# Kernel tuning notes

Hardware: AMD Instinct MI355X
Metric: run time of the kernel (lower is better)

The kernel has to match this reference:

```python
import jax, jax.numpy as jnp
import numpy as np

D_MODEL = 1024
STATE_DIM = 256


def setup_inputs() -> dict:
    key = jax.random.key(0)
    k_u, k_lam, k_B, k_C = jax.random.split(key, 4)
    u = jax.random.normal(k_u, (4, 4096, D_MODEL), dtype=jnp.float32)
    # log_lambda ~ N(3.0, 0.5^2), matching torch.randn(state_dim)*0.5 + 3.0
    log_lambda = jax.random.normal(k_lam, (STATE_DIM,), dtype=jnp.float32) * 0.5 + 3.0
    # torch Linear weights: B.weight [state_dim, d_model], C.weight [d_model, state_dim]
    B_w = jax.random.normal(k_B, (STATE_DIM, D_MODEL), dtype=jnp.float32) / np.sqrt(D_MODEL)
    C_w = jax.random.normal(k_C, (D_MODEL, STATE_DIM), dtype=jnp.float32) / np.sqrt(STATE_DIM)
    D = jnp.zeros((D_MODEL,), dtype=jnp.float32)
    return {"u": u, "log_lambda": log_lambda, "B_w": B_w, "C_w": C_w, "D": D}


def reference(u, log_lambda, B_w, C_w, D):
    # u: [batch, seq, d_model]
    lam = jax.nn.sigmoid(log_lambda)                      # [state_dim]
    Bu = jnp.einsum('bsd,nd->bsn', u, B_w)                # [batch, seq, state_dim]

    def step(h, bu_t):
        h = lam * h + bu_t                                # [batch, state_dim]
        return h, h

    h0 = jnp.zeros((u.shape[0], lam.shape[0]), dtype=u.dtype)
    # scan over time axis; Bu transposed to [seq, batch, state_dim]
    _, hs = jax.lax.scan(step, h0, jnp.swapaxes(Bu, 0, 1))
    hs = jnp.swapaxes(hs, 0, 1)                           # [batch, seq, state_dim]
    y = jnp.einsum('bsn,dn->bsd', hs, C_w) + D * u        # [batch, seq, d_model]
    return y
```

## Files before the change

### kernel.cpp

```cpp
#include <hip/hip_runtime.h>
#include <math.h>

typedef unsigned short ushort_t;
typedef __bf16 v8bf __attribute__((ext_vector_type(8)));
typedef __bf16 v4bf __attribute__((ext_vector_type(4)));
typedef float  v4f  __attribute__((ext_vector_type(4)));
typedef float  f32x4 __attribute__((ext_vector_type(4)));

#define BATCH 4
#define SEQ 4096
#define DM 1024
#define NS 256
#define MROWS (BATCH*SEQ)

#define NCH 128
#define CL (SEQ/NCH)

#define BK 32
#define BK1 64

typedef __attribute__((address_space(1))) void as1_void;
typedef __attribute__((address_space(3))) void as3_void;

__device__ __forceinline__ void gl_lds16(const void* g, void* l) {
    __builtin_amdgcn_global_load_lds((as1_void*)g, (as3_void*)l, 16, 0, 0);
}

__device__ __forceinline__ ushort_t f2bf(float f) {
    unsigned u = __builtin_bit_cast(unsigned, f);
    u += 0x7fff + ((u >> 16) & 1);
    return (ushort_t)(u >> 16);
}

__device__ __forceinline__ float sigm(float x) { return 1.0f / (1.0f + expf(-x)); }

__device__ __forceinline__ float powk(int e, float l1, float l2, float l4,
                                      float l8, float l16) {
    float w = 1.0f;
    if (e & 1)  w *= l1;
    if (e & 2)  w *= l2;
    if (e & 4)  w *= l4;
    if (e & 8)  w *= l8;
    if (e & 16) w *= l16;
    return w;
}

__global__ __launch_bounds__(256)
void gemm1_fused(const float* __restrict__ A,
                 const ushort_t* __restrict__ B,
                 float* __restrict__ Bu,
                 const float* __restrict__ ll,
                 float* __restrict__ cf)
{
    const int K = DM;
    __shared__ __align__(16) ushort_t As[2][32*BK1];
    __shared__ __align__(16) ushort_t Bs[2][256*BK1];

    const int tid  = threadIdx.x;
    const int lane = tid & 63;
    const int wave = tid >> 6;
    const int m0   = blockIdx.x * 32;

    const int fr = lane & 15;
    const int fq = lane >> 4;

    int arow[2], ac4[2];
    #pragma unroll
    for (int j = 0; j < 2; ++j) {
        int cid = j*256 + tid;
        arow[j] = cid >> 4;
        ac4[j]  = (cid & 15) * 4;
    }
    int brow[8], bc[8];
    #pragma unroll
    for (int j = 0; j < 8; ++j) {
        int cid = j*256 + tid;
        brow[j] = cid >> 3;
        bc[j]   = (cid & 7) * 8;
    }

    f32x4 acc[2][4] = {};
    v4f areg[2];

    #pragma unroll
    for (int j = 0; j < 2; ++j)
        areg[j] = *(const v4f*)&A[(size_t)(m0 + arow[j])*K + ac4[j]];
    #pragma unroll
    for (int j = 0; j < 8; ++j)
        gl_lds16(&B[(size_t)brow[j]*K + bc[j]], &Bs[0][(j*256 + tid)*8]);

    const int NIT = K / BK1;
    for (int it = 0; it < NIT; ++it) {
        const int cur = it & 1;
        #pragma unroll
        for (int j = 0; j < 2; ++j)
            *(v4bf*)&As[cur][arow[j]*BK1 + ac4[j]] = __builtin_convertvector(areg[j], v4bf);
        __syncthreads();

        if (it + 1 < NIT) {
            const int k1 = (it + 1) * BK1;
            #pragma unroll
            for (int j = 0; j < 8; ++j)
                gl_lds16(&B[(size_t)brow[j]*K + k1 + bc[j]], &Bs[cur^1][(j*256 + tid)*8]);
            #pragma unroll
            for (int j = 0; j < 2; ++j)
                areg[j] = *(const v4f*)&A[(size_t)(m0 + arow[j])*K + k1 + ac4[j]];
        }

        #pragma unroll
        for (int kk = 0; kk < 2; ++kk) {
            v8bf af[2], bf[4];
            #pragma unroll
            for (int mi = 0; mi < 2; ++mi)
                af[mi] = *reinterpret_cast<const v8bf*>(
                    &As[cur][(mi*16 + fr)*BK1 + kk*32 + fq*8]);
            #pragma unroll
            for (int ni = 0; ni < 4; ++ni)
                bf[ni] = *reinterpret_cast<const v8bf*>(
                    &Bs[cur][(wave*64 + ni*16 + fr)*BK1 + kk*32 + fq*8]);

            #pragma unroll
            for (int mi = 0; mi < 2; ++mi)
                #pragma unroll
                for (int ni = 0; ni < 4; ++ni)
                    acc[mi][ni] = __builtin_amdgcn_mfma_f32_16x16x32_bf16(
                                      af[mi], bf[ni], acc[mi][ni], 0, 0, 0);
        }
    }

    #pragma unroll
    for (int mi = 0; mi < 2; ++mi) {
        #pragma unroll
        for (int ni = 0; ni < 4; ++ni) {
            const int col = wave*64 + ni*16 + fr;
            #pragma unroll
            for (int r = 0; r < 4; ++r)
                Bu[(size_t)(m0 + mi*16 + fq*4 + r)*NS + col] = acc[mi][ni][r];
        }
    }

    const int b_idx = m0 >> 12;
    const int c_idx = (m0 & 4095) >> 5;

    #pragma unroll
    for (int ni = 0; ni < 4; ++ni) {
        const int col = wave*64 + ni*16 + fr;
        const float l1  = sigm(ll[col]);
        const float l2  = l1*l1;
        const float l4  = l2*l2;
        const float l8  = l4*l4;
        const float l16 = l8*l8;
        float f = 0.0f;
        #pragma unroll
        for (int mi = 0; mi < 2; ++mi) {
            float w = powk(28 - mi*16 - fq*4, l1, l2, l4, l8, l16);
            f = fmaf(w, acc[mi][ni][3], f);
            w *= l1; f = fmaf(w, acc[mi][ni][2], f);
            w *= l1; f = fmaf(w, acc[mi][ni][1], f);
            w *= l1; f = fmaf(w, acc[mi][ni][0], f);
        }
        f += __shfl_xor(f, 16, 64);
        f += __shfl_xor(f, 32, 64);
        if (fq == 0)
            cf[((size_t)b_idx*NCH + c_idx)*NS + col] = f;
    }
}

__global__ __launch_bounds__(256)
void gemm2_mfma(const ushort_t* __restrict__ A,
                const ushort_t* __restrict__ B,
                float* __restrict__ C,
                const float* __restrict__ Dvec, const float* __restrict__ U)
{
    const int K = NS;
    const int N = DM;
    __shared__ __align__(16) ushort_t As[2][128*BK];
    __shared__ __align__(16) ushort_t Bs[2][128*BK];

    const int tid  = threadIdx.x;
    const int lane = tid & 63;
    const int wave = tid >> 6;
    const int wrow = wave >> 1;
    const int wcol = wave & 1;
    const int n0 = blockIdx.x * 128;
    const int m0 = blockIdx.y * 128;

    const int fr = lane & 15;
    const int fq = lane >> 4;

    f32x4 acc[4][4] = {};

    const int ch0 = wave*128 + lane;
    const int ch1 = ch0 + 64;
    const int r0 = ch0 >> 2, c0 = (ch0 & 3) * 8;
    const int r1 = ch1 >> 2, c1 = (ch1 & 3) * 8;

    gl_lds16(&A[(size_t)(m0 + r0)*K + c0], &As[0][ch0*8]);
    gl_lds16(&B[(size_t)(n0 + r0)*K + c0], &Bs[0][ch0*8]);
    gl_lds16(&A[(size_t)(m0 + r1)*K + c1], &As[0][ch1*8]);
    gl_lds16(&B[(size_t)(n0 + r1)*K + c1], &Bs[0][ch1*8]);

    for (int it = 0; it < K/BK; ++it) {
        const int cur = it & 1;
        __syncthreads();

        if (it + 1 < K/BK) {
            const int k1 = (it + 1) * BK;
            gl_lds16(&A[(size_t)(m0 + r0)*K + k1 + c0], &As[cur^1][ch0*8]);
            gl_lds16(&B[(size_t)(n0 + r0)*K + k1 + c0], &Bs[cur^1][ch0*8]);
            gl_lds16(&A[(size_t)(m0 + r1)*K + k1 + c1], &As[cur^1][ch1*8]);
            gl_lds16(&B[(size_t)(n0 + r1)*K + k1 + c1], &Bs[cur^1][ch1*8]);
        }

        v8bf af[4], bf[4];
        #pragma unroll
        for (int mi = 0; mi < 4; ++mi)
            af[mi] = *reinterpret_cast<const v8bf*>(&As[cur][(wrow*64 + mi*16 + fr)*BK + fq*8]);
        #pragma unroll
        for (int ni = 0; ni < 4; ++ni)
            bf[ni] = *reinterpret_cast<const v8bf*>(&Bs[cur][(wcol*64 + ni*16 + fr)*BK + fq*8]);

        #pragma unroll
        for (int mi = 0; mi < 4; ++mi)
            #pragma unroll
            for (int ni = 0; ni < 4; ++ni)
                acc[mi][ni] = __builtin_amdgcn_mfma_f32_16x16x32_bf16(
                                  af[mi], bf[ni], acc[mi][ni], 0, 0, 0);
    }

    const int orow = m0 + wrow*64 + (lane >> 4)*4;
    const int ocol = n0 + wcol*64 + (lane & 15);
    #pragma unroll
    for (int ni = 0; ni < 4; ++ni) {
        const int col = ocol + ni*16;
        const float d = Dvec[col];
        #pragma unroll
        for (int mi = 0; mi < 4; ++mi) {
            #pragma unroll
            for (int r = 0; r < 4; ++r) {
                const size_t idx = (size_t)(orow + mi*16 + r) * N + col;
                float v = acc[mi][ni][r];
                if (d != 0.0f) v = fmaf(d, U[idx], v);
                C[idx] = v;
            }
        }
    }
}

__global__ __launch_bounds__(256)
void cvt_w(const float4* __restrict__ Bw, const float4* __restrict__ Cw,
           ushort_t* __restrict__ Bo, ushort_t* __restrict__ Co)
{
    const int i = blockIdx.x * 256 + threadIdx.x;
    const float4* src = blockIdx.y ? Cw : Bw;
    ushort_t*     dst = blockIdx.y ? Co : Bo;
    float4 v = src[i];
    ushort4 o;
    o.x = f2bf(v.x); o.y = f2bf(v.y); o.z = f2bf(v.z); o.w = f2bf(v.w);
    *(ushort4*)&dst[4*(size_t)i] = o;
}

__global__ __launch_bounds__(256)
void scan_apply(const float* __restrict__ Bu, const float* __restrict__ ll,
                const float* __restrict__ cf, ushort_t* __restrict__ hs16)
{
    const int n = threadIdx.x, c = blockIdx.x, b = blockIdx.y;
    const float lam = sigm(ll[n]);
    float lamL = lam;
    #pragma unroll
    for (int i = 0; i < 5; ++i) lamL *= lamL;

    const float* cfb = cf + (size_t)b*NCH*NS + n;
    float x = 0.0f;
    for (int c0 = 0; c0 < c; c0 += 16) {
        float v[16];
        #pragma unroll
        for (int j = 0; j < 16; ++j) {
            const int cc = c0 + j;
            v[j] = (cc < c) ? cfb[(size_t)cc*NS] : 0.0f;
        }
        #pragma unroll
        for (int j = 0; j < 16; ++j) {
            if (c0 + j < c) x = fmaf(lamL, x, v[j]);
        }
    }

    const size_t base = ((size_t)b*SEQ + (size_t)c*CL)*NS + n;
    float v[CL];
    #pragma unroll
    for (int t = 0; t < CL; ++t)
        v[t] = Bu[base + (size_t)t*NS];

    float h = x;
    #pragma unroll
    for (int t = 0; t < CL; ++t) { h = fmaf(lam, h, v[t]); v[t] = h; }
    #pragma unroll
    for (int t = 0; t < CL; ++t) hs16[base + (size_t)t*NS] = f2bf(v[t]);
}

extern "C" void kernel_launch(void* const* d_in, const int* in_sizes, int n_in,
                              void* d_out, int out_size, void* d_ws, size_t ws_size,
                              hipStream_t stream) {
    const float* u          = (const float*)d_in[0];
    const float* log_lambda = (const float*)d_in[1];
    const float* B_w        = (const float*)d_in[2];
    const float* C_w        = (const float*)d_in[3];
    const float* Dv         = (const float*)d_in[4];
    float* y  = (float*)d_out;

    char* w = (char*)d_ws;
    float*    Bu    = (float*)w;
    ushort_t* hs16  = (ushort_t*)(w + 16777216);
    ushort_t* Bw16  = (ushort_t*)(w + 25165824);
    ushort_t* Cw16  = (ushort_t*)(w + 25690112);
    float*    cf    = (float*)(w + 26214400);

    dim3 blk(256);

    cvt_w<<<dim3(256, 2), blk, 0, stream>>>((const float4*)B_w, (const float4*)C_w,
                                            Bw16, Cw16);

    gemm1_fused<<<dim3(MROWS/32), blk, 0, stream>>>(u, Bw16, Bu, log_lambda, cf);

    scan_apply<<<dim3(NCH, BATCH), blk, 0, stream>>>(Bu, log_lambda, cf, hs16);

    gemm2_mfma<<<dim3(DM/128, MROWS/128), blk, 0, stream>>>(
        hs16, Cw16, y, Dv, u);
}
```

Baseline: 167.8 us.

## Fuse weight conversion, GEMM1 and chunked scan into one cooperative kernel

Merges the weight bf16 conversion, the first GEMM with chunk-carry computation, and the chunked scan into a single cooperative kernel that uses two grid-wide syncs. The Bu intermediate now stays in LDS instead of making a round trip through global memory. Tiles grow to 64 rows with 512 threads, and the LDS layouts are XOR-swizzled to reduce bank conflicts. The risks are grid-sync cost, the need for all 256 blocks to be co-resident, and heavier LDS use that lowers occupancy.

```diff
diff --git a/kernel.cpp b/kernel.cpp
--- a/kernel.cpp
+++ b/kernel.cpp
@@ -1,4 +1,5 @@
 #include <hip/hip_runtime.h>
+#include <hip/hip_cooperative_groups.h>
 #include <math.h>
 
 typedef unsigned short ushort_t;
@@ -16,8 +17,10 @@
 #define NCH 128
 #define CL (SEQ/NCH)
 
+#define BM1 64
+#define BK1 64
 #define BK 32
-#define BK1 64
+#define SST 258
 
 typedef __attribute__((address_space(1))) void as1_void;
 typedef __attribute__((address_space(3))) void as3_void;
@@ -45,38 +48,57 @@
     return w;
 }
 
-__global__ __launch_bounds__(256)
-void gemm1_fused(const float* __restrict__ A,
-                 const ushort_t* __restrict__ B,
-                 float* __restrict__ Bu,
-                 const float* __restrict__ ll,
-                 float* __restrict__ cf)
+__global__ __launch_bounds__(512)
+void fused1(const float* __restrict__ A,
+            const float* __restrict__ BwF,
+            const float* __restrict__ CwF,
+            ushort_t* __restrict__ Bw16,
+            ushort_t* __restrict__ Cw16,
+            const float* __restrict__ ll,
+            float* __restrict__ cf,
+            ushort_t* __restrict__ hs)
 {
     const int K = DM;
-    __shared__ __align__(16) ushort_t As[2][32*BK1];
-    __shared__ __align__(16) ushort_t Bs[2][256*BK1];
+    __shared__ __align__(16) union {
+        struct { ushort_t As[2][BM1*BK1]; ushort_t Bs[2][NS*BK1]; } g;
+        struct { float S[BM1*SST]; } s;
+    } L;
 
     const int tid  = threadIdx.x;
     const int lane = tid & 63;
     const int wave = tid >> 6;
-    const int m0   = blockIdx.x * 32;
-
+    const int wr = wave >> 2;
+    const int wc = wave & 3;
     const int fr = lane & 15;
     const int fq = lane >> 4;
-
-    int arow[2], ac4[2];
+    const int m0 = blockIdx.x * BM1;
+
+    {
+        const int gid = blockIdx.x * 512 + tid;
+        const float4* src = (gid < 65536) ? (const float4*)BwF : (const float4*)CwF;
+        ushort_t*     dst = (gid < 65536) ? Bw16 : Cw16;
+        const int gi = gid & 65535;
+        float4 v = src[gi];
+        ushort4 o;
+        o.x = f2bf(v.x); o.y = f2bf(v.y); o.z = f2bf(v.z); o.w = f2bf(v.w);
+        *(ushort4*)&dst[(size_t)gi*4] = o;
+    }
+    cooperative_groups::this_grid().sync();
+
+    int arow[2], ac4[2], aoff[2];
     #pragma unroll
     for (int j = 0; j < 2; ++j) {
-        int cid = j*256 + tid;
+        int cid = j*512 + tid;
         arow[j] = cid >> 4;
         ac4[j]  = (cid & 15) * 4;
-    }
-    int brow[8], bc[8];
-    #pragma unroll
-    for (int j = 0; j < 8; ++j) {
-        int cid = j*256 + tid;
+        aoff[j] = arow[j]*BK1 + (((ac4[j] >> 3) ^ (arow[j] & 7)) * 8) + (ac4[j] & 4);
+    }
+    int brow[4], bcs[4];
+    #pragma unroll
+    for (int j = 0; j < 4; ++j) {
+        int cid = j*512 + tid;
         brow[j] = cid >> 3;
-        bc[j]   = (cid & 7) * 8;
+        bcs[j]  = (((cid & 7) ^ (brow[j] & 7)) * 8);
     }
 
     f32x4 acc[2][4] = {};
@@ -86,22 +108,23 @@
     for (int j = 0; j < 2; ++j)
         areg[j] = *(const v4f*)&A[(size_t)(m0 + arow[j])*K + ac4[j]];
     #pragma unroll
-    for (int j = 0; j < 8; ++j)
-        gl_lds16(&B[(size_t)brow[j]*K + bc[j]], &Bs[0][(j*256 + tid)*8]);
+    for (int j = 0; j < 4; ++j)
+        gl_lds16(&Bw16[(size_t)brow[j]*K + bcs[j]], &L.g.Bs[0][(j*512 + tid)*8]);
 
     const int NIT = K / BK1;
     for (int it = 0; it < NIT; ++it) {
         const int cur = it & 1;
         #pragma unroll
         for (int j = 0; j < 2; ++j)
-            *(v4bf*)&As[cur][arow[j]*BK1 + ac4[j]] = __builtin_convertvector(areg[j], v4bf);
+            *(v4bf*)&L.g.As[cur][aoff[j]] = __builtin_convertvector(areg[j], v4bf);
         __syncthreads();
 
         if (it + 1 < NIT) {
             const int k1 = (it + 1) * BK1;
             #pragma unroll
-            for (int j = 0; j < 8; ++j)
-                gl_lds16(&B[(size_t)brow[j]*K + k1 + bc[j]], &Bs[cur^1][(j*256 + tid)*8]);
+            for (int j = 0; j < 4; ++j)
+                gl_lds16(&Bw16[(size_t)brow[j]*K + k1 + bcs[j]],
+                         &L.g.Bs[cur^1][(j*512 + tid)*8]);
             #pragma unroll
             for (int j = 0; j < 2; ++j)
                 areg[j] = *(const v4f*)&A[(size_t)(m0 + arow[j])*K + k1 + ac4[j]];
@@ -111,14 +134,17 @@
         for (int kk = 0; kk < 2; ++kk) {
             v8bf af[2], bf[4];
             #pragma unroll
-            for (int mi = 0; mi < 2; ++mi)
-                af[mi] = *reinterpret_cast<const v8bf*>(
-                    &As[cur][(mi*16 + fr)*BK1 + kk*32 + fq*8]);
-            #pragma unroll
-            for (int ni = 0; ni < 4; ++ni)
-                bf[ni] = *reinterpret_cast<const v8bf*>(
-                    &Bs[cur][(wave*64 + ni*16 + fr)*BK1 + kk*32 + fq*8]);
-
+            for (int mi = 0; mi < 2; ++mi) {
+                const int r  = wr*32 + mi*16 + fr;
+                const int ch = (kk*4 + fq) ^ (r & 7);
+                af[mi] = *reinterpret_cast<const v8bf*>(&L.g.As[cur][r*BK1 + ch*8]);
+            }
+            #pragma unroll
+            for (int ni = 0; ni < 4; ++ni) {
+                const int r  = wc*64 + ni*16 + fr;
+                const int ch = (kk*4 + fq) ^ (r & 7);
+                bf[ni] = *reinterpret_cast<const v8bf*>(&L.g.Bs[cur][r*BK1 + ch*8]);
+            }
             #pragma unroll
             for (int mi = 0; mi < 2; ++mi)
                 #pragma unroll
@@ -127,24 +153,24 @@
                                       af[mi], bf[ni], acc[mi][ni], 0, 0, 0);
         }
     }
+    __syncthreads();
 
     #pragma unroll
     for (int mi = 0; mi < 2; ++mi) {
         #pragma unroll
         for (int ni = 0; ni < 4; ++ni) {
-            const int col = wave*64 + ni*16 + fr;
+            const int col = wc*64 + ni*16 + fr;
             #pragma unroll
             for (int r = 0; r < 4; ++r)
-                Bu[(size_t)(m0 + mi*16 + fq*4 + r)*NS + col] = acc[mi][ni][r];
+                L.s.S[(wr*32 + mi*16 + fq*4 + r)*SST + col] = acc[mi][ni][r];
         }
     }
 
     const int b_idx = m0 >> 12;
-    const int c_idx = (m0 & 4095) >> 5;
-
+    const int c0    = (m0 & 4095) >> 5;
     #pragma unroll
     for (int ni = 0; ni < 4; ++ni) {
-        const int col = wave*64 + ni*16 + fr;
+        const int col = wc*64 + ni*16 + fr;
         const float l1  = sigm(ll[col]);
         const float l2  = l1*l1;
         const float l4  = l2*l2;
@@ -162,7 +188,51 @@
         f += __shfl_xor(f, 16, 64);
         f += __shfl_xor(f, 32, 64);
         if (fq == 0)
-            cf[((size_t)b_idx*NCH + c_idx)*NS + col] = f;
+            cf[((size_t)b_idx*NCH + c0 + wr)*NS + col] = f;
+    }
+
+    cooperative_groups::this_grid().sync();
+
+    const int h = tid >> 8;
+    const int n = tid & 255;
+    const int cG = c0 + h;
+    const float lam = sigm(ll[n]);
+    float lamL = lam;
+    #pragma unroll
+    for (int i = 0; i < 5; ++i) lamL *= lamL;
+
+    const float* cfb = cf + (size_t)b_idx*NCH*NS + n;
+    float x = 0.0f;
+    int cc = 0;
+    for (; cc + 16 <= cG; cc += 16) {
+        float vv[16];
+        #pragma unroll
+        for (int j = 0; j < 16; ++j) vv[j] = cfb[(size_t)(cc + j)*NS];
+        #pragma unroll
+        for (int j = 0; j < 16; ++j) x = fmaf(lamL, x, vv[j]);
+    }
+    for (; cc < cG; ++cc) x = fmaf(lamL, x, cfb[(size_t)cc*NS]);
+
+    float v[CL];
+    #pragma unroll
+    for (int t = 0; t < CL; ++t)
+        v[t] = L.s.S[(h*32 + t)*SST + n];
+    float hv = x;
+    #pragma unroll
+    for (int t = 0; t < CL; ++t) { hv = fmaf(lam, hv, v[t]); v[t] = hv; }
+
+    __syncthreads();
+    ushort_t* H = (ushort_t*)&L.s.S[0];
+    #pragma unroll
+    for (int t = 0; t < CL; ++t)
+        H[(h*32 + t)*NS + n] = f2bf(v[t]);
+    __syncthreads();
+
+    ushort_t* hg = hs + (size_t)m0*NS;
+    #pragma unroll
+    for (int j = 0; j < 4; ++j) {
+        const int cid = j*512 + tid;
+        *(uint4*)&hg[(size_t)cid*8] = *(const uint4*)&H[(size_t)cid*8];
     }
 }
 
@@ -247,57 +317,6 @@
     }
 }
 
-__global__ __launch_bounds__(256)
-void cvt_w(const float4* __restrict__ Bw, const float4* __restrict__ Cw,
-           ushort_t* __restrict__ Bo, ushort_t* __restrict__ Co)
-{
-    const int i = blockIdx.x * 256 + threadIdx.x;
-    const float4* src = blockIdx.y ? Cw : Bw;
-    ushort_t*     dst = blockIdx.y ? Co : Bo;
-    float4 v = src[i];
-    ushort4 o;
-    o.x = f2bf(v.x); o.y = f2bf(v.y); o.z = f2bf(v.z); o.w = f2bf(v.w);
-    *(ushort4*)&dst[4*(size_t)i] = o;
-}
-
-__global__ __launch_bounds__(256)
-void scan_apply(const float* __restrict__ Bu, const float* __restrict__ ll,
-                const float* __restrict__ cf, ushort_t* __restrict__ hs16)
-{
-    const int n = threadIdx.x, c = blockIdx.x, b = blockIdx.y;
-    const float lam = sigm(ll[n]);
-    float lamL = lam;
-    #pragma unroll
-    for (int i = 0; i < 5; ++i) lamL *= lamL;
-
-    const float* cfb = cf + (size_t)b*NCH*NS + n;
-    float x = 0.0f;
-    for (int c0 = 0; c0 < c; c0 += 16) {
-        float v[16];
-        #pragma unroll
-        for (int j = 0; j < 16; ++j) {
-            const int cc = c0 + j;
-            v[j] = (cc < c) ? cfb[(size_t)cc*NS] : 0.0f;
-        }
-        #pragma unroll
-        for (int j = 0; j < 16; ++j) {
-            if (c0 + j < c) x = fmaf(lamL, x, v[j]);
-        }
-    }
-
-    const size_t base = ((size_t)b*SEQ + (size_t)c*CL)*NS + n;
-    float v[CL];
-    #pragma unroll
-    for (int t = 0; t < CL; ++t)
-        v[t] = Bu[base + (size_t)t*NS];
-
-    float h = x;
-    #pragma unroll
-    for (int t = 0; t < CL; ++t) { h = fmaf(lam, h, v[t]); v[t] = h; }
-    #pragma unroll
-    for (int t = 0; t < CL; ++t) hs16[base + (size_t)t*NS] = f2bf(v[t]);
-}
-
 extern "C" void kernel_launch(void* const* d_in, const int* in_sizes, int n_in,
                               void* d_out, int out_size, void* d_ws, size_t ws_size,
                               hipStream_t stream) {
@@ -309,21 +328,15 @@
     float* y  = (float*)d_out;
 
     char* w = (char*)d_ws;
-    float*    Bu    = (float*)w;
-    ushort_t* hs16  = (ushort_t*)(w + 16777216);
-    ushort_t* Bw16  = (ushort_t*)(w + 25165824);
-    ushort_t* Cw16  = (ushort_t*)(w + 25690112);
-    float*    cf    = (float*)(w + 26214400);
-
-    dim3 blk(256);
-
-    cvt_w<<<dim3(256, 2), blk, 0, stream>>>((const float4*)B_w, (const float4*)C_w,
-                                            Bw16, Cw16);
-
-    gemm1_fused<<<dim3(MROWS/32), blk, 0, stream>>>(u, Bw16, Bu, log_lambda, cf);
-
-    scan_apply<<<dim3(NCH, BATCH), blk, 0, stream>>>(Bu, log_lambda, cf, hs16);
-
-    gemm2_mfma<<<dim3(DM/128, MROWS/128), blk, 0, stream>>>(
+    ushort_t* hs16 = (ushort_t*)w;
+    ushort_t* Bw16 = (ushort_t*)(w + 8388608);
+    ushort_t* Cw16 = (ushort_t*)(w + 8912896);
+    float*    cf   = (float*)(w + 9437184);
+
+    void* args[] = { (void*)&u, (void*)&B_w, (void*)&C_w, (void*)&Bw16,
+                     (void*)&Cw16, (void*)&log_lambda, (void*)&cf, (void*)&hs16 };
+    hipLaunchCooperativeKernel(fused1, dim3(MROWS/BM1), dim3(512), args, 0, stream);
+
+    gemm2_mfma<<<dim3(DM/128, MROWS/128), dim3(256), 0, stream>>>(
         hs16, Cw16, y, Dv, u);
 }
```

Measured after the change: 226.1 us. 34.7% more time.

## Fuse chunk scan into output GEMM and XOR-swizzle LDS tiles in input GEMM

Applied to the files above, without the earlier changes.

Removes the separate scan_apply kernel and the bf16 hs intermediate buffer. Each 512-thread block of the new gemm2_scan loads a 64-row slab of Bu into LDS, recomputes the chunk carry-in from cf, runs the in-chunk recurrence, and writes bf16 states into a swizzled LDS tile. It then loops over all 8 output column panels, streaming C_w tiles through double buffering. gemm1 also gets XOR-swizzled LDS layouts for A and B to reduce bank conflicts. The cost is that every block recomputes the carry prefix over up to 128 chunks, uses large LDS (about 100KB), and has a smaller per-wave MFMA tile.

```diff
diff --git a/kernel.cpp b/kernel.cpp
--- a/kernel.cpp
+++ b/kernel.cpp
@@ -16,8 +16,9 @@
 #define NCH 128
 #define CL (SEQ/NCH)
 
-#define BK 32
 #define BK1 64
+#define BM2 64
+#define BK2 64
 
 typedef __attribute__((address_space(1))) void as1_void;
 typedef __attribute__((address_space(3))) void as3_void;
@@ -54,7 +55,7 @@
 {
     const int K = DM;
     __shared__ __align__(16) ushort_t As[2][32*BK1];
-    __shared__ __align__(16) ushort_t Bs[2][256*BK1];
+    __shared__ __align__(16) ushort_t Bs[2][NS*BK1];
 
     const int tid  = threadIdx.x;
     const int lane = tid & 63;
@@ -64,19 +65,20 @@
     const int fr = lane & 15;
     const int fq = lane >> 4;
 
-    int arow[2], ac4[2];
+    int arow[2], ac4[2], aoff[2];
     #pragma unroll
     for (int j = 0; j < 2; ++j) {
         int cid = j*256 + tid;
         arow[j] = cid >> 4;
         ac4[j]  = (cid & 15) * 4;
-    }
-    int brow[8], bc[8];
+        aoff[j] = arow[j]*BK1 + (((ac4[j] >> 3) ^ (arow[j] & 7)) * 8) + (ac4[j] & 4);
+    }
+    int brow[8], bcs[8];
     #pragma unroll
     for (int j = 0; j < 8; ++j) {
         int cid = j*256 + tid;
         brow[j] = cid >> 3;
-        bc[j]   = (cid & 7) * 8;
+        bcs[j]  = ((cid & 7) ^ (brow[j] & 7)) * 8;
     }
 
     f32x4 acc[2][4] = {};
@@ -87,21 +89,22 @@
         areg[j] = *(const v4f*)&A[(size_t)(m0 + arow[j])*K + ac4[j]];
     #pragma unroll
     for (int j = 0; j < 8; ++j)
-        gl_lds16(&B[(size_t)brow[j]*K + bc[j]], &Bs[0][(j*256 + tid)*8]);
+        gl_lds16(&B[(size_t)brow[j]*K + bcs[j]], &Bs[0][(j*256 + tid)*8]);
 
     const int NIT = K / BK1;
     for (int it = 0; it < NIT; ++it) {
         const int cur = it & 1;
         #pragma unroll
         for (int j = 0; j < 2; ++j)
-            *(v4bf*)&As[cur][arow[j]*BK1 + ac4[j]] = __builtin_convertvector(areg[j], v4bf);
+            *(v4bf*)&As[cur][aoff[j]] = __builtin_convertvector(areg[j], v4bf);
         __syncthreads();
 
         if (it + 1 < NIT) {
             const int k1 = (it + 1) * BK1;
             #pragma unroll
             for (int j = 0; j < 8; ++j)
-                gl_lds16(&B[(size_t)brow[j]*K + k1 + bc[j]], &Bs[cur^1][(j*256 + tid)*8]);
+                gl_lds16(&B[(size_t)brow[j]*K + k1 + bcs[j]],
+                         &Bs[cur^1][(j*256 + tid)*8]);
             #pragma unroll
             for (int j = 0; j < 2; ++j)
                 areg[j] = *(const v4f*)&A[(size_t)(m0 + arow[j])*K + k1 + ac4[j]];
@@ -111,14 +114,17 @@
         for (int kk = 0; kk < 2; ++kk) {
             v8bf af[2], bf[4];
             #pragma unroll
-            for (int mi = 0; mi < 2; ++mi)
-                af[mi] = *reinterpret_cast<const v8bf*>(
-                    &As[cur][(mi*16 + fr)*BK1 + kk*32 + fq*8]);
-            #pragma unroll
-            for (int ni = 0; ni < 4; ++ni)
-                bf[ni] = *reinterpret_cast<const v8bf*>(
-                    &Bs[cur][(wave*64 + ni*16 + fr)*BK1 + kk*32 + fq*8]);
-
+            for (int mi = 0; mi < 2; ++mi) {
+                const int r  = mi*16 + fr;
+                const int ch = (kk*4 + fq) ^ (r & 7);
+                af[mi] = *reinterpret_cast<const v8bf*>(&As[cur][r*BK1 + ch*8]);
+            }
+            #pragma unroll
+            for (int ni = 0; ni < 4; ++ni) {
+                const int r  = wave*64 + ni*16 + fr;
+                const int ch = (kk*4 + fq) ^ (r & 7);
+                bf[ni] = *reinterpret_cast<const v8bf*>(&Bs[cur][r*BK1 + ch*8]);
+            }
             #pragma unroll
             for (int mi = 0; mi < 2; ++mi)
                 #pragma unroll
@@ -166,85 +172,129 @@
     }
 }
 
-__global__ __launch_bounds__(256)
-void gemm2_mfma(const ushort_t* __restrict__ A,
-                const ushort_t* __restrict__ B,
-                float* __restrict__ C,
-                const float* __restrict__ Dvec, const float* __restrict__ U)
+__global__ __launch_bounds__(512)
+void gemm2_scan(const float* __restrict__ Bu,
+                const ushort_t* __restrict__ Cw,
+                const float* __restrict__ ll,
+                const float* __restrict__ cf,
+                float* __restrict__ Y,
+                const float* __restrict__ Dvec,
+                const float* __restrict__ U)
 {
-    const int K = NS;
-    const int N = DM;
-    __shared__ __align__(16) ushort_t As[2][128*BK];
-    __shared__ __align__(16) ushort_t Bs[2][128*BK];
+    __shared__ __align__(16) float    BuS[BM2*NS];
+    __shared__ __align__(16) ushort_t hsS[BM2*NS];
+    __shared__ __align__(16) ushort_t Bsw[2][128*BK2];
 
     const int tid  = threadIdx.x;
     const int lane = tid & 63;
     const int wave = tid >> 6;
-    const int wrow = wave >> 1;
-    const int wcol = wave & 1;
-    const int n0 = blockIdx.x * 128;
-    const int m0 = blockIdx.y * 128;
-
     const int fr = lane & 15;
     const int fq = lane >> 4;
-
-    f32x4 acc[4][4] = {};
-
-    const int ch0 = wave*128 + lane;
-    const int ch1 = ch0 + 64;
-    const int r0 = ch0 >> 2, c0 = (ch0 & 3) * 8;
-    const int r1 = ch1 >> 2, c1 = (ch1 & 3) * 8;
-
-    gl_lds16(&A[(size_t)(m0 + r0)*K + c0], &As[0][ch0*8]);
-    gl_lds16(&B[(size_t)(n0 + r0)*K + c0], &Bs[0][ch0*8]);
-    gl_lds16(&A[(size_t)(m0 + r1)*K + c1], &As[0][ch1*8]);
-    gl_lds16(&B[(size_t)(n0 + r1)*K + c1], &Bs[0][ch1*8]);
-
-    for (int it = 0; it < K/BK; ++it) {
-        const int cur = it & 1;
-        __syncthreads();
-
-        if (it + 1 < K/BK) {
-            const int k1 = (it + 1) * BK;
-            gl_lds16(&A[(size_t)(m0 + r0)*K + k1 + c0], &As[cur^1][ch0*8]);
-            gl_lds16(&B[(size_t)(n0 + r0)*K + k1 + c0], &Bs[cur^1][ch0*8]);
-            gl_lds16(&A[(size_t)(m0 + r1)*K + k1 + c1], &As[cur^1][ch1*8]);
-            gl_lds16(&B[(size_t)(n0 + r1)*K + k1 + c1], &Bs[cur^1][ch1*8]);
-        }
-
-        v8bf af[4], bf[4];
-        #pragma unroll
-        for (int mi = 0; mi < 4; ++mi)
-            af[mi] = *reinterpret_cast<const v8bf*>(&As[cur][(wrow*64 + mi*16 + fr)*BK + fq*8]);
-        #pragma unroll
-        for (int ni = 0; ni < 4; ++ni)
-            bf[ni] = *reinterpret_cast<const v8bf*>(&Bs[cur][(wcol*64 + ni*16 + fr)*BK + fq*8]);
-
-        #pragma unroll
-        for (int mi = 0; mi < 4; ++mi)
-            #pragma unroll
-            for (int ni = 0; ni < 4; ++ni)
-                acc[mi][ni] = __builtin_amdgcn_mfma_f32_16x16x32_bf16(
-                                  af[mi], bf[ni], acc[mi][ni], 0, 0, 0);
-    }
-
-    const int orow = m0 + wrow*64 + (lane >> 4)*4;
-    const int ocol = n0 + wcol*64 + (lane & 15);
-    #pragma unroll
-    for (int ni = 0; ni < 4; ++ni) {
-        const int col = ocol + ni*16;
-        const float d = Dvec[col];
-        #pragma unroll
-        for (int mi = 0; mi < 4; ++mi) {
-            #pragma unroll
-            for (int r = 0; r < 4; ++r) {
-                const size_t idx = (size_t)(orow + mi*16 + r) * N + col;
-                float v = acc[mi][ni][r];
-                if (d != 0.0f) v = fmaf(d, U[idx], v);
-                C[idx] = v;
+    const int wm = wave >> 2;
+    const int nq = wave & 3;
+    const int m0 = blockIdx.x * BM2;
+
+    const float* bsrc = Bu + (size_t)m0*NS;
+    #pragma unroll
+    for (int j = 0; j < 8; ++j)
+        gl_lds16(bsrc + (j*512 + tid)*4, &BuS[(j*512 + tid)*4]);
+
+    const int br2 = (tid >> 3) & 127;
+    #define STAGE_B(g, buf)                                                    \
+        {                                                                      \
+            const int p_ = (g) >> 2, ks_ = (g) & 3;                            \
+            _Pragma("unroll")                                                  \
+            for (int jj = 0; jj < 2; ++jj) {                                   \
+                const int cid = jj*512 + tid;                                  \
+                const int row_ = cid >> 3, kch_ = cid & 7;                     \
+                const int koff_ = ks_*BK2 + ((kch_ ^ (row_ & 7)) * 8);         \
+                gl_lds16(&Cw[(size_t)(p_*128 + row_)*NS + koff_],              \
+                         &Bsw[buf][cid*8]);                                    \
+            }                                                                  \
+        }
+    STAGE_B(0, 0);
+
+    const int h2 = tid >> 8;
+    const int n  = tid & 255;
+    const int b_idx = m0 >> 12;
+    const int cG = ((m0 & 4095) >> 5) + h2;
+    const float lam = sigm(ll[n]);
+    float lamL = lam;
+    #pragma unroll
+    for (int i = 0; i < 5; ++i) lamL *= lamL;
+
+    const float* cfb = cf + (size_t)b_idx*NCH*NS + n;
+    float x = 0.0f;
+    int cc = 0;
+    for (; cc + 16 <= cG; cc += 16) {
+        float vv[16];
+        #pragma unroll
+        for (int j = 0; j < 16; ++j) vv[j] = cfb[(size_t)(cc + j)*NS];
+        #pragma unroll
+        for (int j = 0; j < 16; ++j) x = fmaf(lamL, x, vv[j]);
+    }
+    for (; cc < cG; ++cc) x = fmaf(lamL, x, cfb[(size_t)cc*NS]);
+
+    __syncthreads();
+
+    float h = x;
+    #pragma unroll
+    for (int t = 0; t < CL; ++t) {
+        const int row = h2*32 + t;
+        h = fmaf(lam, h, BuS[row*NS + n]);
+        hsS[row*NS + (((n >> 3) ^ (row & 7)) << 3) + (n & 7)] = f2bf(h);
+    }
+    __syncthreads();
+
+    int g = 0;
+    for (int p = 0; p < 8; ++p) {
+        f32x4 acc[2][2] = {};
+        for (int ks = 0; ks < 4; ++ks, ++g) {
+            const int cur = g & 1;
+            if (g) __syncthreads();
+            if (g + 1 < 32) STAGE_B(g + 1, cur ^ 1);
+
+            #pragma unroll
+            for (int kk = 0; kk < 2; ++kk) {
+                v8bf af[2], bf[2];
+                #pragma unroll
+                for (int mi = 0; mi < 2; ++mi) {
+                    const int r  = wm*32 + mi*16 + fr;
+                    const int ch = (ks*8 + kk*4 + fq) ^ (r & 7);
+                    af[mi] = *reinterpret_cast<const v8bf*>(&hsS[r*NS + ch*8]);
+                }
+                #pragma unroll
+                for (int ni = 0; ni < 2; ++ni) {
+                    const int rn = nq*32 + ni*16 + fr;
+                    const int ch = (kk*4 + fq) ^ (rn & 7);
+                    bf[ni] = *reinterpret_cast<const v8bf*>(&Bsw[cur][rn*BK2 + ch*8]);
+                }
+                #pragma unroll
+                for (int mi = 0; mi < 2; ++mi)
+                    #pragma unroll
+                    for (int ni = 0; ni < 2; ++ni)
+                        acc[mi][ni] = __builtin_amdgcn_mfma_f32_16x16x32_bf16(
+                                          af[mi], bf[ni], acc[mi][ni], 0, 0, 0);
             }
         }
-    }
+        #pragma unroll
+        for (int ni = 0; ni < 2; ++ni) {
+            const int gcol = p*128 + nq*32 + ni*16 + fr;
+            const float d = Dvec[gcol];
+            #pragma unroll
+            for (int mi = 0; mi < 2; ++mi) {
+                #pragma unroll
+                for (int r = 0; r < 4; ++r) {
+                    const int grow = m0 + wm*32 + mi*16 + fq*4 + r;
+                    const size_t idx = (size_t)grow*DM + gcol;
+                    float v = acc[mi][ni][r];
+                    if (d != 0.0f) v = fmaf(d, U[idx], v);
+                    Y[idx] = v;
+                }
+            }
+        }
+    }
+    #undef STAGE_B
 }
 
 __global__ __launch_bounds__(256)
@@ -260,44 +310,6 @@
     *(ushort4*)&dst[4*(size_t)i] = o;
 }
 
-__global__ __launch_bounds__(256)
-void scan_apply(const float* __restrict__ Bu, const float* __restrict__ ll,
-                const float* __restrict__ cf, ushort_t* __restrict__ hs16)
-{
-    const int n = threadIdx.x, c = blockIdx.x, b = blockIdx.y;
-    const float lam = sigm(ll[n]);
-    float lamL = lam;
-    #pragma unroll
-    for (int i = 0; i < 5; ++i) lamL *= lamL;
-
-    const float* cfb = cf + (size_t)b*NCH*NS + n;
-    float x = 0.0f;
-    for (int c0 = 0; c0 < c; c0 += 16) {
-        float v[16];
-        #pragma unroll
-        for (int j = 0; j < 16; ++j) {
-            const int cc = c0 + j;
-            v[j] = (cc < c) ? cfb[(size_t)cc*NS] : 0.0f;
-        }
-        #pragma unroll
-        for (int j = 0; j < 16; ++j) {
-            if (c0 + j < c) x = fmaf(lamL, x, v[j]);
-        }
-    }
-
-    const size_t base = ((size_t)b*SEQ + (size_t)c*CL)*NS + n;
-    float v[CL];
-    #pragma unroll
-    for (int t = 0; t < CL; ++t)
-        v[t] = Bu[base + (size_t)t*NS];
-
-    float h = x;
-    #pragma unroll
-    for (int t = 0; t < CL; ++t) { h = fmaf(lam, h, v[t]); v[t] = h; }
-    #pragma unroll
-    for (int t = 0; t < CL; ++t) hs16[base + (size_t)t*NS] = f2bf(v[t]);
-}
-
 extern "C" void kernel_launch(void* const* d_in, const int* in_sizes, int n_in,
                               void* d_out, int out_size, void* d_ws, size_t ws_size,
                               hipStream_t stream) {
@@ -309,11 +321,10 @@
     float* y  = (float*)d_out;
 
     char* w = (char*)d_ws;
-    float*    Bu    = (float*)w;
-    ushort_t* hs16  = (ushort_t*)(w + 16777216);
-    ushort_t* Bw16  = (ushort_t*)(w + 25165824);
-    ushort_t* Cw16  = (ushort_t*)(w + 25690112);
-    float*    cf    = (float*)(w + 26214400);
+    float*    Bu   = (float*)w;
+    ushort_t* Bw16 = (ushort_t*)(w + 16777216);
+    ushort_t* Cw16 = (ushort_t*)(w + 17301504);
+    float*    cf   = (float*)(w + 17825792);
 
     dim3 blk(256);
 
@@ -322,8 +333,6 @@
 
     gemm1_fused<<<dim3(MROWS/32), blk, 0, stream>>>(u, Bw16, Bu, log_lambda, cf);
 
-    scan_apply<<<dim3(NCH, BATCH), blk, 0, stream>>>(Bu, log_lambda, cf, hs16);
-
-    gemm2_mfma<<<dim3(DM/128, MROWS/128), blk, 0, stream>>>(
-        hs16, Cw16, y, Dv, u);
-}
+    gemm2_scan<<<dim3(MROWS/BM2), dim3(512), 0, stream>>>(
+        Bu, Cw16, log_lambda, cf, y, Dv, u);
+}
```

Result: faster. 163.7 us (-2.5%).
